# Performance work log

Hardware: AMD Instinct MI355X
Metric: run time of the kernel (lower is better)

The kernel has to match this reference:

```python
import jax, jax.numpy as jnp
import numpy as np

N, L, WD, PD, FS, NF, C = 1024, 128, 300, 50, 3, 512, 53
V, PV = 100000, 256          # word vocab, position-feature vocab
D = WD + 2 * PD              # 400: concat token representation width
LP = L - FS + 1              # 126: conv output length (valid conv)
NEG = jnp.float32(-1e30)


def setup_inputs() -> dict:
    key = jax.random.key(0)
    ks = jax.random.split(key, 11)
    tokens = jax.random.randint(ks[0], (N, L), 0, V, dtype=jnp.int32)
    pf1 = jax.random.randint(ks[1], (N, L), 0, PV, dtype=jnp.int32)
    pf2 = jax.random.randint(ks[2], (N, L), 0, PV, dtype=jnp.int32)
    # entity positions in conv-output coordinates, sorted so p1 <= p2 < LP
    entity_pos = jnp.sort(jax.random.randint(ks[3], (N, 2), 0, LP, dtype=jnp.int32), axis=1)
    wordvec = jax.random.normal(ks[4], (V, WD), jnp.float32) * 0.02
    pf1_emb = jax.random.normal(ks[5], (PV, PD), jnp.float32) * 0.02
    pf2_emb = jax.random.normal(ks[6], (PV, PD), jnp.float32) * 0.02
    conv_w = jax.random.normal(ks[7], (NF, FS, D), jnp.float32) * (1.0 / np.sqrt(FS * D))
    conv_b = jnp.zeros((NF,), jnp.float32)
    out_w = jax.random.normal(ks[8], (3 * NF, C), jnp.float32) * (1.0 / np.sqrt(3 * NF))
    out_b = jnp.zeros((C,), jnp.float32)
    return dict(tokens=tokens, pf1=pf1, pf2=pf2, entity_pos=entity_pos,
                wordvec=wordvec, pf1_emb=pf1_emb, pf2_emb=pf2_emb,
                conv_w=conv_w, conv_b=conv_b, out_w=out_w, out_b=out_b)


def reference(tokens, pf1, pf2, entity_pos, wordvec, pf1_emb, pf2_emb,
              conv_w, conv_b, out_w, out_b):
    # token representation: [N, L, D]
    x = jnp.concatenate([wordvec[tokens], pf1_emb[pf1], pf2_emb[pf2]], axis=-1)
    # valid conv over seq with kernel spanning full feature width -> matmul form
    win = jnp.stack([x[:, k:k + LP, :] for k in range(FS)], axis=2)  # [N, LP, FS, D]
    conv = jnp.tanh(jnp.einsum('ntkd,fkd->ntf', win, conv_w) + conv_b)  # [N, LP, NF]
    # piecewise (3-segment) max pool keyed on entity positions
    idx = jnp.arange(LP)[None, :]                      # [1, LP]
    p1 = entity_pos[:, 0:1]                            # [N, 1]
    p2 = entity_pos[:, 1:2]
    m1 = idx <= p1                                     # [0, p1]
    m2 = (idx >= p1) & (idx <= p2)                     # [p1, p2]
    m3 = idx >= p2                                     # [p2, LP)
    masks = jnp.stack([m1, m2, m3], axis=1)            # [N, 3, LP]
    pooled = jnp.max(jnp.where(masks[:, :, :, None], conv[:, None, :, :], NEG), axis=2)  # [N, 3, NF]
    # torch code: cat(pool1,pool2,pool3) -> [3,F], transpose -> [F,3], flatten
    feat = jnp.transpose(pooled, (0, 2, 1)).reshape(N, 3 * NF)  # [N, 3*NF]
    return feat @ out_w + out_b                        # [N, C]
```

## Files before the change

### kernel.cpp

```cpp
#include <hip/hip_runtime.h>


#define XSTRIDE 424
#define XROWS 131
#define LPV 126
#define NC 53

typedef __attribute__((ext_vector_type(8))) short short8;
typedef __attribute__((ext_vector_type(4))) float floatx4;

__device__ __forceinline__ unsigned short f2bf_rne(float x) {
    unsigned u = __float_as_uint(x);
    u += 0x7fffu + ((u >> 16) & 1u);
    return (unsigned short)(u >> 16);
}

__global__ void __launch_bounds__(1024)
prep(const float* __restrict__ convw, const float* __restrict__ outw,
     unsigned short* __restrict__ convwb2, float* __restrict__ outwT) {
    int i = blockIdx.x * 1024 + threadIdx.x;
    if (i < 622592) {
        int e = i & 7, col = (i >> 3) & 15, kq = (i >> 7) & 3;
        int rest = i >> 9;
        int ks = rest % 38, ftile = rest / 38;
        int k = ks * 32 + kq * 8 + e, f = ftile * 16 + col;
        convwb2[i] = (k < 1200) ? f2bf_rne(convw[f * 1200 + k])
                                : (unsigned short)0;
    } else {
        int i2 = i - 622592;
        if (i2 < 81408) {
            int c = i2 / 1536, j = i2 - c * 1536;
            outwT[i2] = outw[j * 53 + c];
        }
    }
}

extern "C" __global__ void __launch_bounds__(1024)
pcnn_fused(const int* __restrict__ tokens, const int* __restrict__ pf1,
           const int* __restrict__ pf2, const int* __restrict__ epos,
           const float* __restrict__ wordvec,
           const float* __restrict__ pf1e,
           const float* __restrict__ pf2e,
           const unsigned short* __restrict__ convwb2,
           const float* __restrict__ convb,
           const float* __restrict__ outwT,
           const float* __restrict__ outb,
           float* __restrict__ out)
{
    extern __shared__ char smem[];
    unsigned short* xl = (unsigned short*)smem;
    float* pfeat = (float*)(smem + 111088);
    int*   idx   = (int*)(smem + 111088 + 12288);

    const int n    = blockIdx.x;
    const int tid  = threadIdx.x;
    const int lane = tid & 63;
    const int wv   = tid >> 6;
    const int wr   = wv & 1;
    const int wc   = wv >> 1;

    if (tid < 128) {
        int base = n * 128 + tid;
        idx[tid]       = tokens[base];
        idx[128 + tid] = pf1[base];
        idx[256 + tid] = pf2[base];
    }
    {
        const short8 z8 = {0, 0, 0, 0, 0, 0, 0, 0};
        short8* dst = (short8*)xl;
        for (int i = tid; i < 159; i += 1024) {
            int row = 128 + i / 53, c = i % 53;
            dst[row * 53 + c] = z8;
        }
    }
    __syncthreads();

    {
        const float2* wv2 = (const float2*)wordvec;
        const float2* p12 = (const float2*)pf1e;
        const float2* p22 = (const float2*)pf2e;
        #pragma unroll 4
        for (int i = tid; i < 128 * 150; i += 1024) {
            int row = i / 150, c = i - row * 150;
            float2 v = wv2[(long)idx[row] * 150 + c];
            *(ushort2*)(xl + row * XSTRIDE + 2 * c) =
                make_ushort2(f2bf_rne(v.x), f2bf_rne(v.y));
        }
        #pragma unroll 4
        for (int i = tid; i < 128 * 25; i += 1024) {
            int row = i / 25, c = i - row * 25;
            float2 v = p12[idx[128 + row] * 25 + c];
            *(ushort2*)(xl + row * XSTRIDE + 300 + 2 * c) =
                make_ushort2(f2bf_rne(v.x), f2bf_rne(v.y));
            float2 w = p22[idx[256 + row] * 25 + c];
            *(ushort2*)(xl + row * XSTRIDE + 350 + 2 * c) =
                make_ushort2(f2bf_rne(w.x), f2bf_rne(w.y));
        }
    }
    __syncthreads();

    const int col = lane & 15;
    const int kq  = lane >> 4;

    const floatx4 fz = {0.f, 0.f, 0.f, 0.f};
    floatx4 acc[4][4];
    #pragma unroll
    for (int mt = 0; mt < 4; ++mt)
        #pragma unroll
        for (int jt = 0; jt < 4; ++jt) acc[mt][jt] = fz;

    int ck   = kq * 8;
    int aoff = (wr * 64 + col) * XSTRIDE + kq * 8;
    const unsigned short* bb = convwb2 + (wc * 4) * (38 * 512) + lane * 8;

    #pragma unroll 1
    for (int ks = 0; ks < 38; ++ks) {
        short8 b[4], a[4];
        #pragma unroll
        for (int jt = 0; jt < 4; ++jt)
            b[jt] = *(const short8*)(bb + jt * (38 * 512) + ks * 512);
        #pragma unroll
        for (int mt = 0; mt < 4; ++mt)
            a[mt] = *(const short8*)(xl + aoff + mt * (16 * XSTRIDE));
        __builtin_amdgcn_s_setprio(1);
        #pragma unroll
        for (int mt = 0; mt < 4; ++mt)
            #pragma unroll
            for (int jt = 0; jt < 4; ++jt)
                acc[mt][jt] = __builtin_amdgcn_mfma_f32_16x16x32_bf16(
                    a[mt], b[jt], acc[mt][jt], 0, 0, 0);
        __builtin_amdgcn_s_setprio(0);
        ck += 32; aoff += 32;
        if (ck >= 400) { ck -= 400; aoff += XSTRIDE - 400; }
    }

    const int p1 = epos[2 * n], p2 = epos[2 * n + 1];
    #pragma unroll
    for (int jt = 0; jt < 4; ++jt) {
        float m0 = -1e30f, m1 = -1e30f, m2 = -1e30f;
        #pragma unroll
        for (int mt = 0; mt < 4; ++mt) {
            #pragma unroll
            for (int r = 0; r < 4; ++r) {
                int t = wr * 64 + mt * 16 + kq * 4 + r;
                float v = acc[mt][jt][r];
                if (t < LPV) {
                    if (t <= p1) m0 = fmaxf(m0, v);
                    if (t >= p1 && t <= p2) m1 = fmaxf(m1, v);
                    if (t >= p2) m2 = fmaxf(m2, v);
                }
            }
        }
        m0 = fmaxf(m0, __shfl_xor(m0, 16)); m0 = fmaxf(m0, __shfl_xor(m0, 32));
        m1 = fmaxf(m1, __shfl_xor(m1, 16)); m1 = fmaxf(m1, __shfl_xor(m1, 32));
        m2 = fmaxf(m2, __shfl_xor(m2, 16)); m2 = fmaxf(m2, __shfl_xor(m2, 32));
        if (kq == 0) {
            int f = wc * 64 + jt * 16 + col;
            pfeat[wr * 1536 + 3 * f + 0] = m0;
            pfeat[wr * 1536 + 3 * f + 1] = m1;
            pfeat[wr * 1536 + 3 * f + 2] = m2;
        }
    }
    __syncthreads();

    for (int i = tid; i < 1536; i += 1024) {
        float v = fmaxf(pfeat[i], pfeat[1536 + i]);
        int f = i / 3;
        pfeat[i] = tanhf(v + convb[f]);
    }
    __syncthreads();

    {
        const float* feat = pfeat;
        for (int cc = wv; cc < NC; cc += 16) {
            const float* wrow = outwT + cc * 1536;
            float s = 0.f;
            #pragma unroll 4
            for (int jj = lane; jj < 1536; jj += 64)
                s += feat[jj] * wrow[jj];
            s += __shfl_xor(s, 32); s += __shfl_xor(s, 16);
            s += __shfl_xor(s, 8);  s += __shfl_xor(s, 4);
            s += __shfl_xor(s, 2);  s += __shfl_xor(s, 1);
            if (lane == 0) out[n * 53 + cc] = s + outb[cc];
        }
    }
}

extern "C" void kernel_launch(void* const* d_in, const int* in_sizes, int n_in,
                              void* d_out, int out_size, void* d_ws, size_t ws_size,
                              hipStream_t stream) {
    (void)in_sizes; (void)n_in; (void)ws_size; (void)out_size;
    const int* tokens = (const int*)d_in[0];
    const int* pf1    = (const int*)d_in[1];
    const int* pf2    = (const int*)d_in[2];
    const int* epos   = (const int*)d_in[3];
    const float* wordvec = (const float*)d_in[4];
    const float* pf1e    = (const float*)d_in[5];
    const float* pf2e    = (const float*)d_in[6];
    const float* convw   = (const float*)d_in[7];
    const float* convb   = (const float*)d_in[8];
    const float* outw    = (const float*)d_in[9];
    const float* outb    = (const float*)d_in[10];
    float* out = (float*)d_out;

    unsigned short* convwb2 = (unsigned short*)d_ws;
    float* outwT = (float*)((char*)d_ws + 1245184);

    prep<<<dim3(688), dim3(1024), 0, stream>>>(convw, outw, convwb2, outwT);

    const size_t lds_bytes = 111088 + 12288 + 1536;
    pcnn_fused<<<dim3(1024), dim3(1024), lds_bytes, stream>>>(
        tokens, pf1, pf2, epos, wordvec, pf1e, pf2e, convwb2,
        convb, outwT, outb, out);
}
```

Measured before the change: 376.1 us.

## Split fused PCNN kernel into half-sequence blocks plus separate output kernel

Each sample is now handled by two 512-thread blocks, one per half of the sequence, instead of one 1024-thread block. This shrinks LDS per block to about 57KB so more blocks fit per CU, which raises occupancy and lets gather and MFMA phases of different blocks overlap. Partial pooled features go to a global workspace, and a new small kernel combines them, applies tanh and does the output projection. The split adds global round trips and an extra launch, and the halves reload overlapping rows and weight tiles. The word-embedding gather also moves from float2 to float4 loads.

```diff
diff --git a/kernel.cpp b/kernel.cpp
--- a/kernel.cpp
+++ b/kernel.cpp
@@ -2,7 +2,6 @@
 
 
 #define XSTRIDE 424
-#define XROWS 131
 #define LPV 126
 #define NC 53
 
@@ -35,64 +34,64 @@
     }
 }
 
-extern "C" __global__ void __launch_bounds__(1024)
-pcnn_fused(const int* __restrict__ tokens, const int* __restrict__ pf1,
-           const int* __restrict__ pf2, const int* __restrict__ epos,
-           const float* __restrict__ wordvec,
-           const float* __restrict__ pf1e,
-           const float* __restrict__ pf2e,
-           const unsigned short* __restrict__ convwb2,
-           const float* __restrict__ convb,
-           const float* __restrict__ outwT,
-           const float* __restrict__ outb,
-           float* __restrict__ out)
+extern "C" __global__ void __launch_bounds__(512, 4)
+pcnn_half(const int* __restrict__ tokens, const int* __restrict__ pf1,
+          const int* __restrict__ pf2, const int* __restrict__ epos,
+          const float* __restrict__ wordvec,
+          const float* __restrict__ pf1e,
+          const float* __restrict__ pf2e,
+          const unsigned short* __restrict__ convwb2,
+          float* __restrict__ pfe)
 {
     extern __shared__ char smem[];
     unsigned short* xl = (unsigned short*)smem;
-    float* pfeat = (float*)(smem + 111088);
-    int*   idx   = (int*)(smem + 111088 + 12288);
-
-    const int n    = blockIdx.x;
+    int* idx = (int*)(smem + 56816);
+
+    const int bid = blockIdx.x;
+    const int n   = bid >> 1;
+    const int wr  = bid & 1;
+    const int r0  = wr * 64;
+    const int nreal = wr ? 64 : 67;
+
     const int tid  = threadIdx.x;
     const int lane = tid & 63;
     const int wv   = tid >> 6;
-    const int wr   = wv & 1;
-    const int wc   = wv >> 1;
-
-    if (tid < 128) {
-        int base = n * 128 + tid;
+
+    if (tid < nreal) {
+        int base = n * 128 + r0 + tid;
         idx[tid]       = tokens[base];
-        idx[128 + tid] = pf1[base];
-        idx[256 + tid] = pf2[base];
-    }
-    {
+        idx[67 + tid]  = pf1[base];
+        idx[134 + tid] = pf2[base];
+    }
+    if (wr) {
         const short8 z8 = {0, 0, 0, 0, 0, 0, 0, 0};
         short8* dst = (short8*)xl;
-        for (int i = tid; i < 159; i += 1024) {
-            int row = 128 + i / 53, c = i % 53;
+        for (int i = tid; i < 159; i += 512) {
+            int row = 64 + i / 53, c = i % 53;
             dst[row * 53 + c] = z8;
         }
     }
     __syncthreads();
 
     {
-        const float2* wv2 = (const float2*)wordvec;
+        const float4* wv4 = (const float4*)wordvec;
         const float2* p12 = (const float2*)pf1e;
         const float2* p22 = (const float2*)pf2e;
         #pragma unroll 4
-        for (int i = tid; i < 128 * 150; i += 1024) {
-            int row = i / 150, c = i - row * 150;
-            float2 v = wv2[(long)idx[row] * 150 + c];
-            *(ushort2*)(xl + row * XSTRIDE + 2 * c) =
-                make_ushort2(f2bf_rne(v.x), f2bf_rne(v.y));
+        for (int i = tid; i < nreal * 75; i += 512) {
+            int row = i / 75, c = i - row * 75;
+            float4 v = wv4[(long)idx[row] * 75 + c];
+            *(ushort4*)(xl + row * XSTRIDE + 4 * c) =
+                make_ushort4(f2bf_rne(v.x), f2bf_rne(v.y),
+                             f2bf_rne(v.z), f2bf_rne(v.w));
         }
         #pragma unroll 4
-        for (int i = tid; i < 128 * 25; i += 1024) {
+        for (int i = tid; i < nreal * 25; i += 512) {
             int row = i / 25, c = i - row * 25;
-            float2 v = p12[idx[128 + row] * 25 + c];
+            float2 v = p12[idx[67 + row] * 25 + c];
             *(ushort2*)(xl + row * XSTRIDE + 300 + 2 * c) =
                 make_ushort2(f2bf_rne(v.x), f2bf_rne(v.y));
-            float2 w = p22[idx[256 + row] * 25 + c];
+            float2 w = p22[idx[134 + row] * 25 + c];
             *(ushort2*)(xl + row * XSTRIDE + 350 + 2 * c) =
                 make_ushort2(f2bf_rne(w.x), f2bf_rne(w.y));
         }
@@ -110,15 +109,15 @@
         for (int jt = 0; jt < 4; ++jt) acc[mt][jt] = fz;
 
     int ck   = kq * 8;
-    int aoff = (wr * 64 + col) * XSTRIDE + kq * 8;
-    const unsigned short* bb = convwb2 + (wc * 4) * (38 * 512) + lane * 8;
+    int aoff = col * XSTRIDE + kq * 8;
+    const unsigned short* bb = convwb2 + lane * 8;
 
     #pragma unroll 1
     for (int ks = 0; ks < 38; ++ks) {
         short8 b[4], a[4];
         #pragma unroll
         for (int jt = 0; jt < 4; ++jt)
-            b[jt] = *(const short8*)(bb + jt * (38 * 512) + ks * 512);
+            b[jt] = *(const short8*)(bb + ((wv * 4 + jt) * 38 + ks) * 512);
         #pragma unroll
         for (int mt = 0; mt < 4; ++mt)
             a[mt] = *(const short8*)(xl + aoff + mt * (16 * XSTRIDE));
@@ -135,6 +134,7 @@
     }
 
     const int p1 = epos[2 * n], p2 = epos[2 * n + 1];
+    float* pf_out = pfe + (n * 2 + wr) * 1536;
     #pragma unroll
     for (int jt = 0; jt < 4; ++jt) {
         float m0 = -1e30f, m1 = -1e30f, m2 = -1e30f;
@@ -142,12 +142,12 @@
         for (int mt = 0; mt < 4; ++mt) {
             #pragma unroll
             for (int r = 0; r < 4; ++r) {
-                int t = wr * 64 + mt * 16 + kq * 4 + r;
+                int gt = r0 + mt * 16 + kq * 4 + r;
                 float v = acc[mt][jt][r];
-                if (t < LPV) {
-                    if (t <= p1) m0 = fmaxf(m0, v);
-                    if (t >= p1 && t <= p2) m1 = fmaxf(m1, v);
-                    if (t >= p2) m2 = fmaxf(m2, v);
+                if (gt < LPV) {
+                    if (gt <= p1) m0 = fmaxf(m0, v);
+                    if (gt >= p1 && gt <= p2) m1 = fmaxf(m1, v);
+                    if (gt >= p2) m2 = fmaxf(m2, v);
                 }
             }
         }
@@ -155,34 +155,43 @@
         m1 = fmaxf(m1, __shfl_xor(m1, 16)); m1 = fmaxf(m1, __shfl_xor(m1, 32));
         m2 = fmaxf(m2, __shfl_xor(m2, 16)); m2 = fmaxf(m2, __shfl_xor(m2, 32));
         if (kq == 0) {
-            int f = wc * 64 + jt * 16 + col;
-            pfeat[wr * 1536 + 3 * f + 0] = m0;
-            pfeat[wr * 1536 + 3 * f + 1] = m1;
-            pfeat[wr * 1536 + 3 * f + 2] = m2;
-        }
+            int f = wv * 64 + jt * 16 + col;
+            pf_out[3 * f + 0] = m0;
+            pf_out[3 * f + 1] = m1;
+            pf_out[3 * f + 2] = m2;
+        }
+    }
+}
+
+extern "C" __global__ void __launch_bounds__(256)
+pcnn_out(const float* __restrict__ pfe, const float* __restrict__ convb,
+         const float* __restrict__ outwT,
+         const float* __restrict__ outb, float* __restrict__ out)
+{
+    __shared__ float feat[1536];
+    const int n = blockIdx.x;
+    const int tid = threadIdx.x;
+    const float* pa = pfe + n * 3072;
+    const float* pb = pa + 1536;
+
+    for (int i = tid; i < 1536; i += 256) {
+        float v = fmaxf(pa[i], pb[i]);
+        feat[i] = tanhf(v + convb[i / 3]);
     }
     __syncthreads();
 
-    for (int i = tid; i < 1536; i += 1024) {
-        float v = fmaxf(pfeat[i], pfeat[1536 + i]);
-        int f = i / 3;
-        pfeat[i] = tanhf(v + convb[f]);
-    }
-    __syncthreads();
-
-    {
-        const float* feat = pfeat;
-        for (int cc = wv; cc < NC; cc += 16) {
-            const float* wrow = outwT + cc * 1536;
-            float s = 0.f;
-            #pragma unroll 4
-            for (int jj = lane; jj < 1536; jj += 64)
-                s += feat[jj] * wrow[jj];
-            s += __shfl_xor(s, 32); s += __shfl_xor(s, 16);
-            s += __shfl_xor(s, 8);  s += __shfl_xor(s, 4);
-            s += __shfl_xor(s, 2);  s += __shfl_xor(s, 1);
-            if (lane == 0) out[n * 53 + cc] = s + outb[cc];
-        }
+    const int lane = tid & 63;
+    const int wv   = tid >> 6;
+    for (int cc = wv; cc < NC; cc += 4) {
+        const float* wrow = outwT + cc * 1536;
+        float s = 0.f;
+        #pragma unroll 4
+        for (int jj = lane; jj < 1536; jj += 64)
+            s += feat[jj] * wrow[jj];
+        s += __shfl_xor(s, 32); s += __shfl_xor(s, 16);
+        s += __shfl_xor(s, 8);  s += __shfl_xor(s, 4);
+        s += __shfl_xor(s, 2);  s += __shfl_xor(s, 1);
+        if (lane == 0) out[n * 53 + cc] = s + outb[cc];
     }
 }
 
@@ -205,11 +214,13 @@
 
     unsigned short* convwb2 = (unsigned short*)d_ws;
     float* outwT = (float*)((char*)d_ws + 1245184);
+    float* pfe   = (float*)((char*)d_ws + 1570816);
 
     prep<<<dim3(688), dim3(1024), 0, stream>>>(convw, outw, convwb2, outwT);
 
-    const size_t lds_bytes = 111088 + 12288 + 1536;
-    pcnn_fused<<<dim3(1024), dim3(1024), lds_bytes, stream>>>(
-        tokens, pf1, pf2, epos, wordvec, pf1e, pf2e, convwb2,
-        convb, outwT, outb, out);
-}
+    const size_t lds_bytes = 56816 + 816;
+    pcnn_half<<<dim3(2048), dim3(512), lds_bytes, stream>>>(
+        tokens, pf1, pf2, epos, wordvec, pf1e, pf2e, convwb2, pfe);
+
+    pcnn_out<<<dim3(1024), dim3(256), 0, stream>>>(pfe, convb, outwT, outb, out);
+}
```

Measured after the change: 362.4 us. 1.04x faster.

## Stage conv weights into LDS via async global_load_lds each k-step

Applied to the files above, without the earlier changes.

Conv weights are now cooperatively streamed into an LDS buffer using global_load_lds once per k-step. Before, each wave read its own B fragments from global memory, and pairs of waves fetched the same data. The prep kernel reorders the weights so each k-step slab is contiguous. The word-embedding gather widens to float4 loads, and the LDS row stride shrinks to make room. The cost is two workgroup barriers per k-step on a single-buffered slab, which limits overlap between the load and the MFMAs.

```diff
diff --git a/kernel.cpp b/kernel.cpp
--- a/kernel.cpp
+++ b/kernel.cpp
@@ -1,8 +1,10 @@
 #include <hip/hip_runtime.h>
 
 
-#define XSTRIDE 424
-#define XROWS 131
+#define XSTRIDE 408
+#define XL_BYTES 106896
+#define BST_OFF  106896
+#define IDX_OFF  139664
 #define LPV 126
 #define NC 53
 
@@ -15,16 +17,24 @@
     return (unsigned short)(u >> 16);
 }
 
+__device__ __forceinline__ void gload_lds16(const void* g, void* l) {
+    __builtin_amdgcn_global_load_lds(
+        (const __attribute__((address_space(1))) void*)g,
+        (__attribute__((address_space(3))) void*)l, 16, 0, 0);
+}
+
 __global__ void __launch_bounds__(1024)
 prep(const float* __restrict__ convw, const float* __restrict__ outw,
-     unsigned short* __restrict__ convwb2, float* __restrict__ outwT) {
+     unsigned short* __restrict__ convwb3, float* __restrict__ outwT) {
     int i = blockIdx.x * 1024 + threadIdx.x;
     if (i < 622592) {
-        int e = i & 7, col = (i >> 3) & 15, kq = (i >> 7) & 3;
-        int rest = i >> 9;
-        int ks = rest % 38, ftile = rest / 38;
-        int k = ks * 32 + kq * 8 + e, f = ftile * 16 + col;
-        convwb2[i] = (k < 1200) ? f2bf_rne(convw[f * 1200 + k])
+        int ks = i >> 14;
+        int r  = i & 16383;
+        int sl = r >> 9;
+        int q  = r & 511;
+        int kq = q >> 7, col = (q >> 3) & 15, e = q & 7;
+        int k = ks * 32 + kq * 8 + e, f = sl * 16 + col;
+        convwb3[i] = (k < 1200) ? f2bf_rne(convw[f * 1200 + k])
                                 : (unsigned short)0;
     } else {
         int i2 = i - 622592;
@@ -35,29 +45,37 @@
     }
 }
 
-extern "C" __global__ void __launch_bounds__(1024)
-pcnn_fused(const int* __restrict__ tokens, const int* __restrict__ pf1,
-           const int* __restrict__ pf2, const int* __restrict__ epos,
-           const float* __restrict__ wordvec,
-           const float* __restrict__ pf1e,
-           const float* __restrict__ pf2e,
-           const unsigned short* __restrict__ convwb2,
-           const float* __restrict__ convb,
-           const float* __restrict__ outwT,
-           const float* __restrict__ outb,
-           float* __restrict__ out)
+extern "C" __global__ void __launch_bounds__(1024, 4)
+pcnn_conv(const int* __restrict__ tokens, const int* __restrict__ pf1,
+          const int* __restrict__ pf2, const int* __restrict__ epos,
+          const float* __restrict__ wordvec,
+          const float* __restrict__ pf1e,
+          const float* __restrict__ pf2e,
+          const unsigned short* __restrict__ convwb3,
+          const float* __restrict__ convb,
+          const float* __restrict__ outwT,
+          const float* __restrict__ outb,
+          float* __restrict__ out)
 {
     extern __shared__ char smem[];
-    unsigned short* xl = (unsigned short*)smem;
-    float* pfeat = (float*)(smem + 111088);
-    int*   idx   = (int*)(smem + 111088 + 12288);
+    unsigned short* xl  = (unsigned short*)smem;
+    unsigned short* bst = (unsigned short*)(smem + BST_OFF);
+    float* pfeat        = (float*)(smem + BST_OFF);
+    int*   idx          = (int*)(smem + IDX_OFF);
 
     const int n    = blockIdx.x;
     const int tid  = threadIdx.x;
     const int lane = tid & 63;
     const int wv   = tid >> 6;
-    const int wr   = wv & 1;
-    const int wc   = wv >> 1;
+    const int wvf  = wv & 7;
+    const int wr   = wv >> 3;
+    const int r0   = wr * 64;
+
+    {
+        const unsigned short* g0 = convwb3 + (2 * wv) * 512 + lane * 8;
+        gload_lds16(g0,       bst + (2 * wv) * 512);
+        gload_lds16(g0 + 512, bst + (2 * wv + 1) * 512);
+    }
 
     if (tid < 128) {
         int base = n * 128 + tid;
@@ -68,23 +86,24 @@
     {
         const short8 z8 = {0, 0, 0, 0, 0, 0, 0, 0};
         short8* dst = (short8*)xl;
-        for (int i = tid; i < 159; i += 1024) {
-            int row = 128 + i / 53, c = i % 53;
-            dst[row * 53 + c] = z8;
-        }
-    }
-    __syncthreads();
-
-    {
-        const float2* wv2 = (const float2*)wordvec;
+        for (int i = tid; i < 153; i += 1024) {
+            int row = 128 + i / 51, c = i % 51;
+            dst[row * 51 + c] = z8;
+        }
+    }
+    __syncthreads();
+
+    {
+        const float4* wv4 = (const float4*)wordvec;
         const float2* p12 = (const float2*)pf1e;
         const float2* p22 = (const float2*)pf2e;
         #pragma unroll 4
-        for (int i = tid; i < 128 * 150; i += 1024) {
-            int row = i / 150, c = i - row * 150;
-            float2 v = wv2[(long)idx[row] * 150 + c];
-            *(ushort2*)(xl + row * XSTRIDE + 2 * c) =
-                make_ushort2(f2bf_rne(v.x), f2bf_rne(v.y));
+        for (int i = tid; i < 128 * 75; i += 1024) {
+            int row = i / 75, c = i - row * 75;
+            float4 v = wv4[(long)idx[row] * 75 + c];
+            *(ushort4*)(xl + row * XSTRIDE + 4 * c) =
+                make_ushort4(f2bf_rne(v.x), f2bf_rne(v.y),
+                             f2bf_rne(v.z), f2bf_rne(v.w));
         }
         #pragma unroll 4
         for (int i = tid; i < 128 * 25; i += 1024) {
@@ -110,18 +129,31 @@
         for (int jt = 0; jt < 4; ++jt) acc[mt][jt] = fz;
 
     int ck   = kq * 8;
-    int aoff = (wr * 64 + col) * XSTRIDE + kq * 8;
-    const unsigned short* bb = convwb2 + (wc * 4) * (38 * 512) + lane * 8;
+    int aoff = (r0 + col) * XSTRIDE + kq * 8;
+    const unsigned short* brd = bst + (wvf * 4) * 512 + lane * 8;
+    unsigned short* l0 = bst + (2 * wv) * 512;
+    unsigned short* l1 = l0 + 512;
 
     #pragma unroll 1
     for (int ks = 0; ks < 38; ++ks) {
         short8 b[4], a[4];
         #pragma unroll
         for (int jt = 0; jt < 4; ++jt)
-            b[jt] = *(const short8*)(bb + jt * (38 * 512) + ks * 512);
+            b[jt] = *(const short8*)(brd + jt * 512);
         #pragma unroll
         for (int mt = 0; mt < 4; ++mt)
             a[mt] = *(const short8*)(xl + aoff + mt * (16 * XSTRIDE));
+        asm volatile("s_waitcnt lgkmcnt(0)" ::: "memory");
+        __builtin_amdgcn_sched_barrier(0);
+        __builtin_amdgcn_s_barrier();
+        __builtin_amdgcn_sched_barrier(0);
+        {
+            int ksn = (ks < 37) ? ks + 1 : 37;
+            const unsigned short* g0 =
+                convwb3 + ksn * 16384 + (2 * wv) * 512 + lane * 8;
+            gload_lds16(g0,       l0);
+            gload_lds16(g0 + 512, l1);
+        }
         __builtin_amdgcn_s_setprio(1);
         #pragma unroll
         for (int mt = 0; mt < 4; ++mt)
@@ -130,6 +162,10 @@
                 acc[mt][jt] = __builtin_amdgcn_mfma_f32_16x16x32_bf16(
                     a[mt], b[jt], acc[mt][jt], 0, 0, 0);
         __builtin_amdgcn_s_setprio(0);
+        asm volatile("s_waitcnt vmcnt(0)" ::: "memory");
+        __builtin_amdgcn_sched_barrier(0);
+        __builtin_amdgcn_s_barrier();
+        __builtin_amdgcn_sched_barrier(0);
         ck += 32; aoff += 32;
         if (ck >= 400) { ck -= 400; aoff += XSTRIDE - 400; }
     }
@@ -142,12 +178,12 @@
         for (int mt = 0; mt < 4; ++mt) {
             #pragma unroll
             for (int r = 0; r < 4; ++r) {
-                int t = wr * 64 + mt * 16 + kq * 4 + r;
+                int gt = r0 + mt * 16 + kq * 4 + r;
                 float v = acc[mt][jt][r];
-                if (t < LPV) {
-                    if (t <= p1) m0 = fmaxf(m0, v);
-                    if (t >= p1 && t <= p2) m1 = fmaxf(m1, v);
-                    if (t >= p2) m2 = fmaxf(m2, v);
+                if (gt < LPV) {
+                    if (gt <= p1) m0 = fmaxf(m0, v);
+                    if (gt >= p1 && gt <= p2) m1 = fmaxf(m1, v);
+                    if (gt >= p2) m2 = fmaxf(m2, v);
                 }
             }
         }
@@ -155,7 +191,7 @@
         m1 = fmaxf(m1, __shfl_xor(m1, 16)); m1 = fmaxf(m1, __shfl_xor(m1, 32));
         m2 = fmaxf(m2, __shfl_xor(m2, 16)); m2 = fmaxf(m2, __shfl_xor(m2, 32));
         if (kq == 0) {
-            int f = wc * 64 + jt * 16 + col;
+            int f = wvf * 64 + jt * 16 + col;
             pfeat[wr * 1536 + 3 * f + 0] = m0;
             pfeat[wr * 1536 + 3 * f + 1] = m1;
             pfeat[wr * 1536 + 3 * f + 2] = m2;
@@ -165,8 +201,7 @@
 
     for (int i = tid; i < 1536; i += 1024) {
         float v = fmaxf(pfeat[i], pfeat[1536 + i]);
-        int f = i / 3;
-        pfeat[i] = tanhf(v + convb[f]);
+        pfeat[i] = tanhf(v + convb[i / 3]);
     }
     __syncthreads();
 
@@ -203,13 +238,13 @@
     const float* outb    = (const float*)d_in[10];
     float* out = (float*)d_out;
 
-    unsigned short* convwb2 = (unsigned short*)d_ws;
+    unsigned short* convwb3 = (unsigned short*)d_ws;
     float* outwT = (float*)((char*)d_ws + 1245184);
 
-    prep<<<dim3(688), dim3(1024), 0, stream>>>(convw, outw, convwb2, outwT);
-
-    const size_t lds_bytes = 111088 + 12288 + 1536;
-    pcnn_fused<<<dim3(1024), dim3(1024), lds_bytes, stream>>>(
-        tokens, pf1, pf2, epos, wordvec, pf1e, pf2e, convwb2,
+    prep<<<dim3(688), dim3(1024), 0, stream>>>(convw, outw, convwb3, outwT);
+
+    const size_t lds_bytes = 141200;
+    pcnn_conv<<<dim3(1024), dim3(1024), lds_bytes, stream>>>(
+        tokens, pf1, pf2, epos, wordvec, pf1e, pf2e, convwb3,
         convb, outwT, outb, out);
 }
```

New measurement: 412.9 us. 1.1x slower.
